# Performance work log

Hardware: AMD Instinct MI355X
Metric: run time of the kernel (lower is better)

## Reference

```python
import jax, jax.numpy as jnp
import numpy as np

B, F, V, K, D, H = 16384, 26, 100000, 16, 13, 400
IN_DIM = F * K + D  # 429
EPS = 1e-5


def _bn(x, g, b):
    # BatchNorm1d in training mode: batch statistics (biased var, like torch)
    m = jnp.mean(x, axis=0)
    v = jnp.mean((x - m) ** 2, axis=0)
    return g * (x - m) / jnp.sqrt(v + EPS) + b


def setup_inputs() -> dict:
    key = jax.random.key(0)
    ks = jax.random.split(key, 12)
    X_cat = jax.random.randint(ks[0], (B, F), 0, V)
    X_dense = jax.random.normal(ks[1], (B, D), dtype=jnp.float32)
    fm1_tables = jax.random.normal(ks[2], (F, V, 1), dtype=jnp.float32) * 0.01
    emb_tables = jax.random.normal(ks[3], (F, V, K), dtype=jnp.float32) * 0.01
    Wd = jax.random.normal(ks[4], (D, 1), dtype=jnp.float32) * 0.1
    bd = jnp.zeros((1,), jnp.float32)
    W1 = jax.random.normal(ks[5], (IN_DIM, H), dtype=jnp.float32) * (1.0 / np.sqrt(IN_DIM))
    b1 = jnp.zeros((H,), jnp.float32)
    g1 = jnp.ones((H,), jnp.float32)
    be1 = jnp.zeros((H,), jnp.float32)
    W2 = jax.random.normal(ks[6], (H, H), dtype=jnp.float32) * (1.0 / np.sqrt(H))
    b2 = jnp.zeros((H,), jnp.float32)
    g2 = jnp.ones((H,), jnp.float32)
    be2 = jnp.zeros((H,), jnp.float32)
    W3 = jax.random.normal(ks[7], (H, 1), dtype=jnp.float32) * (1.0 / np.sqrt(H))
    b3 = jnp.zeros((1,), jnp.float32)
    return dict(X_cat=X_cat, X_dense=X_dense, fm1_tables=fm1_tables,
                emb_tables=emb_tables, Wd=Wd, bd=bd, W1=W1, b1=b1, g1=g1,
                be1=be1, W2=W2, b2=b2, g2=g2, be2=be2, W3=W3, b3=b3)


def reference(X_cat, X_dense, fm1_tables, emb_tables, Wd, bd,
              W1, b1, g1, be1, W2, b2, g2, be2, W3, b3):
    gather = jax.vmap(lambda tab, idx: tab[idx], in_axes=(0, 1), out_axes=1)
    # 1st order: [B, F, 1] -> sum over fields -> [B, 1]
    y_1st = jnp.sum(gather(fm1_tables, X_cat), axis=1) + X_dense @ Wd + bd
    # 2nd order embeddings: [B, F, K]
    emb = gather(emb_tables, X_cat)
    s = jnp.sum(emb, axis=1)                 # [B, K]
    ix = s ** 2 - jnp.sum(emb ** 2, axis=1)  # [B, K]
    fm_y = 0.5 * jnp.sum(ix, axis=1, keepdims=True)
    # DNN on [flattened embeddings, dense]
    x = jnp.concatenate([emb.reshape(emb.shape[0], -1), X_dense], axis=1)
    h = jax.nn.relu(_bn(x @ W1 + b1, g1, be1))
    h = jax.nn.relu(_bn(h @ W2 + b2, g2, be2))
    dnn_y = h @ W3 + b3
    return y_1st + fm_y + dnn_y
```

## Files before the change

kernel.cpp:

```cpp
#include <hip/hip_runtime.h>
#include <stdint.h>

#define B_ROWS 16384
#define NF 26
#define NV 100000
#define ND 13
#define NH 400
#define XPAD 448
#define ZPAD 416
#define EPS 1e-5f

typedef __attribute__((ext_vector_type(8))) short short8;
typedef __attribute__((ext_vector_type(4))) float f32x4;
typedef __attribute__((ext_vector_type(4))) unsigned int uint4v;

__device__ inline float bf2f(unsigned short u) {
    union { unsigned int i; float f; } v; v.i = (unsigned int)u << 16; return v.f;
}
__device__ inline unsigned short f2bf(float f) {
    union { float f; unsigned int i; } v; v.f = f;
    unsigned int r = (v.i + 0x7fff + ((v.i >> 16) & 1)) >> 16;
    return (unsigned short)r;
}

typedef __attribute__((address_space(1))) const unsigned int g_u32;
typedef __attribute__((address_space(3))) unsigned int l_u32;
__device__ __forceinline__ void gload_lds16(const void* g, void* l) {
    __builtin_amdgcn_global_load_lds((g_u32*)g, (l_u32*)l, 16, 0, 0);
}

#define X_OFF    0
#define Z1_OFF   14680064
#define W1S_OFF  28311552
#define W2S_OFF  28712960
#define BASE_OFF 29085696
#define ST_OFF   29151232

__global__ __launch_bounds__(256) void gather_prep(
    const int* __restrict__ Xcat, const float* __restrict__ Xdense,
    const float* __restrict__ fm1, const float* __restrict__ emb,
    const float* __restrict__ Wd, const float* __restrict__ bd,
    const float* __restrict__ W1, const float* __restrict__ W2,
    unsigned short* __restrict__ X, float* __restrict__ base,
    unsigned short* __restrict__ W1s, unsigned short* __restrict__ W2s,
    float* __restrict__ st)
{
    int tid = threadIdx.x;
    if (blockIdx.x >= 1024) {
        int c = (blockIdx.x - 1024) * 256 + tid;
        if (c < 256) {
            for (int i = tid; i < 1664; i += 256) st[i] = 0.f;
        }
        const float* W; unsigned short* dst; int K; int cc;
        if (c < 25088) { W = W1; dst = W1s; K = 429; cc = c; }
        else           { W = W2; dst = W2s; K = 400; cc = c - 25088; }
        int n  = cc % 448;
        int q  = (cc / 448) & 3;
        int kt = cc / 1792;
        unsigned short o[8];
        #pragma unroll
        for (int j = 0; j < 8; ++j) {
            int k = kt * 32 + q * 8 + j;
            float v = (n < NH && k < K) ? W[(size_t)k * NH + n] : 0.f;
            o[j] = f2bf(v);
        }
        *(uint4v*)(dst + (size_t)cc * 8) = *(uint4v*)o;
        return;
    }
    int r = blockIdx.x * 16 + (tid >> 4);
    int k = tid & 15;
    const int* idxp = Xcat + (size_t)r * NF;
    unsigned short* xrow = X + (size_t)r * XPAD;

    float s = 0.f, ss = 0.f;
    #pragma unroll
    for (int f = 0; f < NF; ++f) {
        int idx = idxp[f];
        float v = emb[((size_t)f * NV + idx) * 16 + k];
        s += v; ss += v * v;
        xrow[f * 16 + k] = f2bf(v);
    }
    float fmsum = fm1[(size_t)k * NV + idxp[k]];
    if (k < NF - 16) fmsum += fm1[(size_t)(k + 16) * NV + idxp[k + 16]];
    float dsum = 0.f;
    if (k < ND) {
        float xd = Xdense[(size_t)r * ND + k];
        dsum = xd * Wd[k];
        xrow[NF * 16 + k] = f2bf(xd);
    }
    xrow[429 + k] = 0;
    if (k < 3) xrow[445 + k] = 0;

    float ix = s * s - ss;
    float rf = fmsum, rd = dsum;
    #pragma unroll
    for (int off = 8; off; off >>= 1) {
        ix += __shfl_xor(ix, off, 16);
        rf += __shfl_xor(rf, off, 16);
        rd += __shfl_xor(rd, off, 16);
    }
    if (k == 0) base[r] = 0.5f * ix + rf + rd + bd[0];
}

template<int NT, int LDA, bool APPLY_BN>
__global__ __launch_bounds__(512, 2) void mfma_gemm(
    const unsigned short* __restrict__ A,
    const unsigned short* __restrict__ Wst,
    const float* __restrict__ bias,
    const float* __restrict__ gsumIn, const float* __restrict__ gsqIn,
    const float* __restrict__ g, const float* __restrict__ be,
    unsigned short* __restrict__ Z, int ldz,
    float* __restrict__ gsum, float* __restrict__ gsq)
{
    __shared__ unsigned short b_s[2][14336];
    __shared__ float sredS[4][416];
    __shared__ float sredQ[4][416];
    __shared__ float alpha_s[416], beta_s[416];

    const int tid = threadIdx.x;
    const int lane = tid & 63;
    const int wv = tid >> 6;
    const int rowgrp = wv & 3;
    const int nhalf = wv >> 2;
    const int l15 = lane & 15;
    const int qh = lane >> 4;
    const int m0 = blockIdx.x * 64;
    const int arow = m0 + rowgrp * 16 + l15;
    const int c0 = nhalf * 208;
    const int NFRAG = nhalf ? 12 : 13;

    if constexpr (APPLY_BN) {
        for (int c = tid; c < ZPAD; c += 512) {
            float a = 0.f, b = 0.f;
            if (c < NH) {
                float mean = gsumIn[c] * (1.f / B_ROWS);
                float var  = gsqIn[c] * (1.f / B_ROWS) - mean * mean;
                a = g[c] * rsqrtf(var + EPS);
                b = be[c] - mean * a;
            }
            alpha_s[c] = a; beta_s[c] = b;
        }
    }

    f32x4 acc[13];
    #pragma unroll
    for (int i = 0; i < 13; ++i) acc[i] = f32x4{0.f, 0.f, 0.f, 0.f};

    auto stage = [&](int kt, int buf) {
        #pragma unroll
        for (int i = 0; i < 4; ++i) {
            int cchunk = wv * 256 + i * 64 + lane;
            gload_lds16(Wst + (size_t)kt * 14336 + (size_t)cchunk * 8,
                        &b_s[buf][(size_t)(wv * 256 + i * 64) * 8]);
        }
    };

    if (wv < 7) stage(0, 0);
    short8 af_next = *(const short8*)(A + (size_t)arow * LDA + qh * 8);
    __syncthreads();

    for (int kt = 0; kt < NT; ++kt) {
        if (kt + 1 < NT && wv < 7) stage(kt + 1, (kt + 1) & 1);

        short8 af = af_next;
        if (kt + 1 < NT)
            af_next = *(const short8*)(A + (size_t)arow * LDA + (kt + 1) * 32 + qh * 8);

        if constexpr (APPLY_BN) {
            const int k0 = kt * 32 + qh * 8;
            #pragma unroll
            for (int j = 0; j < 8; ++j) {
                float f = bf2f((unsigned short)af[j]);
                f = fmaxf(0.f, alpha_s[k0 + j] * f + beta_s[k0 + j]);
                af[j] = (short)f2bf(f);
            }
        }
        const unsigned short* bb = &b_s[kt & 1][(size_t)(qh * 448 + c0 + l15) * 8];
        #pragma unroll
        for (int nn = 0; nn < 13; ++nn) {
            if (nn < NFRAG) {
                short8 bf = *(const short8*)(bb + nn * 128);
                acc[nn] = __builtin_amdgcn_mfma_f32_16x16x32_bf16(af, bf, acc[nn], 0, 0, 0);
            }
        }
        __syncthreads();
    }

    #pragma unroll
    for (int nn = 0; nn < 13; ++nn) {
        if (nn < NFRAG) {
            int col = c0 + nn * 16 + l15;
            float bv = bias[col];
            float ps = 0.f, pq = 0.f;
            #pragma unroll
            for (int q = 0; q < 4; ++q) {
                float v = acc[nn][q] + bv;
                ps += v; pq += v * v;
                Z[(size_t)(m0 + rowgrp * 16 + qh * 4 + q) * ldz + col] = f2bf(v);
            }
            ps += __shfl_xor(ps, 16, 64); ps += __shfl_xor(ps, 32, 64);
            pq += __shfl_xor(pq, 16, 64); pq += __shfl_xor(pq, 32, 64);
            if (lane < 16) { sredS[rowgrp][col] = ps; sredQ[rowgrp][col] = pq; }
        }
    }
    if (nhalf == 1) {
        int col = NH + l15;
        if (col < ldz) {
            #pragma unroll
            for (int q = 0; q < 4; ++q)
                Z[(size_t)(m0 + rowgrp * 16 + qh * 4 + q) * ldz + col] = 0;
        }
    }
    __syncthreads();
    for (int c = tid; c < NH; c += 512) {
        float s = sredS[0][c] + sredS[1][c] + sredS[2][c] + sredS[3][c];
        float q = sredQ[0][c] + sredQ[1][c] + sredQ[2][c] + sredQ[3][c];
        atomicAdd(&gsum[c], s);
        atomicAdd(&gsq[c], q);
    }
}

__global__ __launch_bounds__(256) void final_kernel(
    const unsigned short* __restrict__ Z2,
    const float* __restrict__ gsum2, const float* __restrict__ gsq2,
    const float* __restrict__ g2, const float* __restrict__ be2,
    const float* __restrict__ W3, const float* __restrict__ b3,
    const float* __restrict__ base, float* __restrict__ out)
{
    __shared__ float a2s[NH], b2s[NH], w3s[NH];
    int tid = threadIdx.x;
    for (int c = tid; c < NH; c += 256) {
        float mean = gsum2[c] * (1.f / B_ROWS);
        float var  = gsq2[c] * (1.f / B_ROWS) - mean * mean;
        float a = g2[c] * rsqrtf(var + EPS);
        a2s[c] = a;
        b2s[c] = be2[c] - mean * a;
        w3s[c] = W3[c];
    }
    __syncthreads();
    int lane = tid & 63;
    int wv = tid >> 6;
    bool act = lane < 50;
    int cb = lane * 8;
    float al[8], bb[8], w3[8];
    #pragma unroll
    for (int j = 0; j < 8; ++j) {
        al[j] = act ? a2s[cb + j] : 0.f;
        bb[j] = act ? b2s[cb + j] : 0.f;
        w3[j] = act ? w3s[cb + j] : 0.f;
    }
    int r0 = blockIdx.x * 32 + wv * 8;
    float bias3 = b3[0];
    for (int t = 0; t < 8; t += 2) {
        int r = r0 + t;
        float acc0 = 0.f, acc1 = 0.f;
        if (act) {
            short8 z0 = *(const short8*)(Z2 + (size_t)r * ZPAD + cb);
            short8 z1 = *(const short8*)(Z2 + (size_t)(r + 1) * ZPAD + cb);
            #pragma unroll
            for (int j = 0; j < 8; ++j) {
                acc0 += fmaxf(0.f, al[j] * bf2f((unsigned short)z0[j]) + bb[j]) * w3[j];
                acc1 += fmaxf(0.f, al[j] * bf2f((unsigned short)z1[j]) + bb[j]) * w3[j];
            }
        }
        #pragma unroll
        for (int off = 32; off; off >>= 1) {
            acc0 += __shfl_xor(acc0, off, 64);
            acc1 += __shfl_xor(acc1, off, 64);
        }
        if (lane == 0) out[r] = base[r] + acc0 + bias3;
        if (lane == 1) out[r + 1] = base[r + 1] + acc1 + bias3;
    }
}

extern "C" void kernel_launch(void* const* d_in, const int* in_sizes, int n_in,
                              void* d_out, int out_size, void* d_ws, size_t ws_size,
                              hipStream_t stream)
{
    const int*   Xcat = (const int*)d_in[0];
    const float* Xd   = (const float*)d_in[1];
    const float* fm1  = (const float*)d_in[2];
    const float* emb  = (const float*)d_in[3];
    const float* Wd   = (const float*)d_in[4];
    const float* bd   = (const float*)d_in[5];
    const float* W1   = (const float*)d_in[6];
    const float* b1   = (const float*)d_in[7];
    const float* g1   = (const float*)d_in[8];
    const float* be1  = (const float*)d_in[9];
    const float* W2   = (const float*)d_in[10];
    const float* b2   = (const float*)d_in[11];
    const float* g2   = (const float*)d_in[12];
    const float* be2  = (const float*)d_in[13];
    const float* W3   = (const float*)d_in[14];
    const float* b3   = (const float*)d_in[15];

    char* ws = (char*)d_ws;
    unsigned short* X   = (unsigned short*)(ws + X_OFF);
    unsigned short* Z1  = (unsigned short*)(ws + Z1_OFF);
    unsigned short* Z2  = X;
    unsigned short* W1s = (unsigned short*)(ws + W1S_OFF);
    unsigned short* W2s = (unsigned short*)(ws + W2S_OFF);
    float* base = (float*)(ws + BASE_OFF);
    float* st   = (float*)(ws + ST_OFF);
    float* gsum1 = st;          float* gsq1 = st + 416;
    float* gsum2 = st + 832;    float* gsq2 = st + 1248;
    float* out = (float*)d_out;

    gather_prep<<<1213, 256, 0, stream>>>(Xcat, Xd, fm1, emb, Wd, bd, W1, W2,
                                          X, base, W1s, W2s, st);

    mfma_gemm<14, XPAD, false><<<256, 512, 0, stream>>>(
        X, W1s, b1, nullptr, nullptr, nullptr, nullptr, Z1, ZPAD, gsum1, gsq1);

    mfma_gemm<13, ZPAD, true><<<256, 512, 0, stream>>>(
        Z1, W2s, b2, gsum1, gsq1, g1, be1, Z2, ZPAD, gsum2, gsq2);

    final_kernel<<<512, 256, 0, stream>>>(Z2, gsum2, gsq2, g2, be2, W3, b3, base, out);
}
```

Before: 82.52 us.

## Fuse embedding gather into first GEMM, dropping intermediate X buffer

```diff
diff --git a/kernel.cpp b/kernel.cpp
--- a/kernel.cpp
+++ b/kernel.cpp
@@ -29,93 +29,50 @@
     __builtin_amdgcn_global_load_lds((g_u32*)g, (l_u32*)l, 16, 0, 0);
 }
 
-#define X_OFF    0
-#define Z1_OFF   14680064
-#define W1S_OFF  28311552
-#define W2S_OFF  28712960
-#define BASE_OFF 29085696
-#define ST_OFF   29151232
-
-__global__ __launch_bounds__(256) void gather_prep(
-    const int* __restrict__ Xcat, const float* __restrict__ Xdense,
-    const float* __restrict__ fm1, const float* __restrict__ emb,
-    const float* __restrict__ Wd, const float* __restrict__ bd,
+#define Z1_OFF   0
+#define Z2_OFF   13631488
+#define W1S_OFF  27262976
+#define W2S_OFF  27664384
+#define BASE_OFF 28037120
+#define ST_OFF   28102656
+
+__global__ __launch_bounds__(512) void prep_w(
     const float* __restrict__ W1, const float* __restrict__ W2,
-    unsigned short* __restrict__ X, float* __restrict__ base,
     unsigned short* __restrict__ W1s, unsigned short* __restrict__ W2s,
     float* __restrict__ st)
 {
-    int tid = threadIdx.x;
-    if (blockIdx.x >= 1024) {
-        int c = (blockIdx.x - 1024) * 256 + tid;
-        if (c < 256) {
-            for (int i = tid; i < 1664; i += 256) st[i] = 0.f;
-        }
-        const float* W; unsigned short* dst; int K; int cc;
-        if (c < 25088) { W = W1; dst = W1s; K = 429; cc = c; }
-        else           { W = W2; dst = W2s; K = 400; cc = c - 25088; }
-        int n  = cc % 448;
-        int q  = (cc / 448) & 3;
-        int kt = cc / 1792;
-        unsigned short o[8];
-        #pragma unroll
-        for (int j = 0; j < 8; ++j) {
-            int k = kt * 32 + q * 8 + j;
-            float v = (n < NH && k < K) ? W[(size_t)k * NH + n] : 0.f;
-            o[j] = f2bf(v);
-        }
-        *(uint4v*)(dst + (size_t)cc * 8) = *(uint4v*)o;
-        return;
-    }
-    int r = blockIdx.x * 16 + (tid >> 4);
-    int k = tid & 15;
-    const int* idxp = Xcat + (size_t)r * NF;
-    unsigned short* xrow = X + (size_t)r * XPAD;
-
-    float s = 0.f, ss = 0.f;
-    #pragma unroll
-    for (int f = 0; f < NF; ++f) {
-        int idx = idxp[f];
-        float v = emb[((size_t)f * NV + idx) * 16 + k];
-        s += v; ss += v * v;
-        xrow[f * 16 + k] = f2bf(v);
-    }
-    float fmsum = fm1[(size_t)k * NV + idxp[k]];
-    if (k < NF - 16) fmsum += fm1[(size_t)(k + 16) * NV + idxp[k + 16]];
-    float dsum = 0.f;
-    if (k < ND) {
-        float xd = Xdense[(size_t)r * ND + k];
-        dsum = xd * Wd[k];
-        xrow[NF * 16 + k] = f2bf(xd);
-    }
-    xrow[429 + k] = 0;
-    if (k < 3) xrow[445 + k] = 0;
-
-    float ix = s * s - ss;
-    float rf = fmsum, rd = dsum;
-    #pragma unroll
-    for (int off = 8; off; off >>= 1) {
-        ix += __shfl_xor(ix, off, 16);
-        rf += __shfl_xor(rf, off, 16);
-        rd += __shfl_xor(rd, off, 16);
-    }
-    if (k == 0) base[r] = 0.5f * ix + rf + rd + bd[0];
-}
-
-template<int NT, int LDA, bool APPLY_BN>
-__global__ __launch_bounds__(512, 2) void mfma_gemm(
-    const unsigned short* __restrict__ A,
-    const unsigned short* __restrict__ Wst,
-    const float* __restrict__ bias,
-    const float* __restrict__ gsumIn, const float* __restrict__ gsqIn,
-    const float* __restrict__ g, const float* __restrict__ be,
-    unsigned short* __restrict__ Z, int ldz,
+    int c = blockIdx.x * 512 + threadIdx.x;
+    if (blockIdx.x == 0) {
+        for (int i = threadIdx.x; i < 1664; i += 512) st[i] = 0.f;
+    }
+    if (c >= 48384) return;
+    const float* W; unsigned short* dst; int K; int cc;
+    if (c < 25088) { W = W1; dst = W1s; K = 429; cc = c; }
+    else           { W = W2; dst = W2s; K = 400; cc = c - 25088; }
+    int n  = cc % 448;
+    int q  = (cc / 448) & 3;
+    int kt = cc / 1792;
+    unsigned short o[8];
+    #pragma unroll
+    for (int j = 0; j < 8; ++j) {
+        int k = kt * 32 + q * 8 + j;
+        float v = (n < NH && k < K) ? W[(size_t)k * NH + n] : 0.f;
+        o[j] = f2bf(v);
+    }
+    *(uint4v*)(dst + (size_t)cc * 8) = *(uint4v*)o;
+}
+
+__global__ __launch_bounds__(512, 4) void gemm1_fused(
+    const int* __restrict__ Xcat, const float* __restrict__ Xd,
+    const float* __restrict__ fm1, const float* __restrict__ emb,
+    const float* __restrict__ Wd, const float* __restrict__ bd,
+    const unsigned short* __restrict__ Wst, const float* __restrict__ bias,
+    unsigned short* __restrict__ Z, float* __restrict__ base,
     float* __restrict__ gsum, float* __restrict__ gsq)
 {
     __shared__ unsigned short b_s[2][14336];
     __shared__ float sredS[4][416];
     __shared__ float sredQ[4][416];
-    __shared__ float alpha_s[416], beta_s[416];
 
     const int tid = threadIdx.x;
     const int lane = tid & 63;
@@ -129,23 +86,6 @@
     const int c0 = nhalf * 208;
     const int NFRAG = nhalf ? 12 : 13;
 
-    if constexpr (APPLY_BN) {
-        for (int c = tid; c < ZPAD; c += 512) {
-            float a = 0.f, b = 0.f;
-            if (c < NH) {
-                float mean = gsumIn[c] * (1.f / B_ROWS);
-                float var  = gsqIn[c] * (1.f / B_ROWS) - mean * mean;
-                a = g[c] * rsqrtf(var + EPS);
-                b = be[c] - mean * a;
-            }
-            alpha_s[c] = a; beta_s[c] = b;
-        }
-    }
-
-    f32x4 acc[13];
-    #pragma unroll
-    for (int i = 0; i < 13; ++i) acc[i] = f32x4{0.f, 0.f, 0.f, 0.f};
-
     auto stage = [&](int kt, int buf) {
         #pragma unroll
         for (int i = 0; i < 4; ++i) {
@@ -154,36 +94,115 @@
                         &b_s[buf][(size_t)(wv * 256 + i * 64) * 8]);
         }
     };
-
     if (wv < 7) stage(0, 0);
-    short8 af_next = *(const short8*)(A + (size_t)arow * LDA + qh * 8);
+
+    const int* idxp = Xcat + (size_t)arow * NF;
+    const int fpar = qh >> 1;
+    const int khalf = (qh & 1) << 3;
+
+    short8 fr[14];
+    float s8[8] = {0.f,0.f,0.f,0.f,0.f,0.f,0.f,0.f};
+    float ssacc = 0.f;
+    float dsum = 0.f;
+
+    {
+        float v[7][8];
+        #pragma unroll
+        for (int kt = 0; kt < 7; ++kt) {
+            int f = 2 * kt + fpar;
+            int idx = idxp[f];
+            const float* p = emb + (((size_t)f * NV + (size_t)idx) << 4) + khalf;
+            f32x4 x0 = *(const f32x4*)p;
+            f32x4 x1 = *(const f32x4*)(p + 4);
+            v[kt][0]=x0[0]; v[kt][1]=x0[1]; v[kt][2]=x0[2]; v[kt][3]=x0[3];
+            v[kt][4]=x1[0]; v[kt][5]=x1[1]; v[kt][6]=x1[2]; v[kt][7]=x1[3];
+        }
+        #pragma unroll
+        for (int kt = 0; kt < 7; ++kt) {
+            if (nhalf == 0) {
+                #pragma unroll
+                for (int j = 0; j < 8; ++j) { s8[j] += v[kt][j]; ssacc += v[kt][j]*v[kt][j]; }
+            }
+            #pragma unroll
+            for (int j = 0; j < 8; ++j) fr[kt][j] = (short)f2bf(v[kt][j]);
+        }
+    }
+    {
+        float v[7][8];
+        #pragma unroll
+        for (int kt = 7; kt < 13; ++kt) {
+            int f = 2 * kt + fpar;
+            int idx = idxp[f];
+            const float* p = emb + (((size_t)f * NV + (size_t)idx) << 4) + khalf;
+            f32x4 x0 = *(const f32x4*)p;
+            f32x4 x1 = *(const f32x4*)(p + 4);
+            v[kt-7][0]=x0[0]; v[kt-7][1]=x0[1]; v[kt-7][2]=x0[2]; v[kt-7][3]=x0[3];
+            v[kt-7][4]=x1[0]; v[kt-7][5]=x1[1]; v[kt-7][6]=x1[2]; v[kt-7][7]=x1[3];
+        }
+        #pragma unroll
+        for (int j = 0; j < 8; ++j) {
+            int cd = khalf + j;
+            v[6][j] = (qh < 2 && cd < ND) ? Xd[(size_t)arow * ND + cd] : 0.f;
+        }
+        #pragma unroll
+        for (int kt = 7; kt < 13; ++kt) {
+            if (nhalf == 0) {
+                #pragma unroll
+                for (int j = 0; j < 8; ++j) { s8[j] += v[kt-7][j]; ssacc += v[kt-7][j]*v[kt-7][j]; }
+            }
+            #pragma unroll
+            for (int j = 0; j < 8; ++j) fr[kt][j] = (short)f2bf(v[kt-7][j]);
+        }
+        #pragma unroll
+        for (int j = 0; j < 8; ++j) fr[13][j] = (short)f2bf(v[6][j]);
+        if (nhalf == 0 && qh < 2) {
+            #pragma unroll
+            for (int j = 0; j < 8; ++j) {
+                int cd = khalf + j;
+                if (cd < ND) dsum += v[6][j] * Wd[cd];
+            }
+        }
+    }
+    float fmsum = 0.f;
+    if (nhalf == 0) {
+        for (int f = qh; f < NF; f += 4)
+            fmsum += fm1[(size_t)f * NV + idxp[f]];
+    }
+
+    f32x4 acc[13];
+    #pragma unroll
+    for (int i = 0; i < 13; ++i) acc[i] = f32x4{0.f, 0.f, 0.f, 0.f};
+
     __syncthreads();
 
-    for (int kt = 0; kt < NT; ++kt) {
-        if (kt + 1 < NT && wv < 7) stage(kt + 1, (kt + 1) & 1);
-
-        short8 af = af_next;
-        if (kt + 1 < NT)
-            af_next = *(const short8*)(A + (size_t)arow * LDA + (kt + 1) * 32 + qh * 8);
-
-        if constexpr (APPLY_BN) {
-            const int k0 = kt * 32 + qh * 8;
-            #pragma unroll
-            for (int j = 0; j < 8; ++j) {
-                float f = bf2f((unsigned short)af[j]);
-                f = fmaxf(0.f, alpha_s[k0 + j] * f + beta_s[k0 + j]);
-                af[j] = (short)f2bf(f);
-            }
-        }
+    #pragma unroll
+    for (int kt = 0; kt < 14; ++kt) {
+        if (kt + 1 < 14 && wv < 7) stage(kt + 1, (kt + 1) & 1);
         const unsigned short* bb = &b_s[kt & 1][(size_t)(qh * 448 + c0 + l15) * 8];
         #pragma unroll
         for (int nn = 0; nn < 13; ++nn) {
             if (nn < NFRAG) {
                 short8 bf = *(const short8*)(bb + nn * 128);
-                acc[nn] = __builtin_amdgcn_mfma_f32_16x16x32_bf16(af, bf, acc[nn], 0, 0, 0);
+                acc[nn] = __builtin_amdgcn_mfma_f32_16x16x32_bf16(fr[kt], bf, acc[nn], 0, 0, 0);
             }
         }
         __syncthreads();
+    }
+
+    if (nhalf == 0) {
+        float red = 0.f;
+        #pragma unroll
+        for (int j = 0; j < 8; ++j) {
+            float sf = s8[j] + __shfl_xor(s8[j], 32, 64);
+            red += sf * sf;
+        }
+        red -= (ssacc + __shfl_xor(ssacc, 32, 64));
+        red += __shfl_xor(red, 16, 64);
+        float fr2 = fmsum + __shfl_xor(fmsum, 16, 64);
+        fr2 += __shfl_xor(fr2, 32, 64);
+        float dr = dsum + __shfl_xor(dsum, 16, 64);
+        dr += __shfl_xor(dr, 32, 64);
+        if (qh == 0) base[arow] = 0.5f * red + fr2 + dr + bd[0];
     }
 
     #pragma unroll
@@ -196,7 +215,7 @@
             for (int q = 0; q < 4; ++q) {
                 float v = acc[nn][q] + bv;
                 ps += v; pq += v * v;
-                Z[(size_t)(m0 + rowgrp * 16 + qh * 4 + q) * ldz + col] = f2bf(v);
+                Z[(size_t)(m0 + rowgrp * 16 + qh * 4 + q) * ZPAD + col] = f2bf(v);
             }
             ps += __shfl_xor(ps, 16, 64); ps += __shfl_xor(ps, 32, 64);
             pq += __shfl_xor(pq, 16, 64); pq += __shfl_xor(pq, 32, 64);
@@ -205,10 +224,111 @@
     }
     if (nhalf == 1) {
         int col = NH + l15;
-        if (col < ldz) {
-            #pragma unroll
-            for (int q = 0; q < 4; ++q)
-                Z[(size_t)(m0 + rowgrp * 16 + qh * 4 + q) * ldz + col] = 0;
+        #pragma unroll
+        for (int q = 0; q < 4; ++q)
+            Z[(size_t)(m0 + rowgrp * 16 + qh * 4 + q) * ZPAD + col] = 0;
+    }
+    __syncthreads();
+    for (int c = tid; c < NH; c += 512) {
+        float s = sredS[0][c] + sredS[1][c] + sredS[2][c] + sredS[3][c];
+        float q = sredQ[0][c] + sredQ[1][c] + sredQ[2][c] + sredQ[3][c];
+        atomicAdd(&gsum[c], s);
+        atomicAdd(&gsq[c], q);
+    }
+}
+
+__global__ __launch_bounds__(512, 2) void mfma_gemm2(
+    const unsigned short* __restrict__ A,
+    const unsigned short* __restrict__ Wst,
+    const float* __restrict__ bias,
+    const float* __restrict__ gsumIn, const float* __restrict__ gsqIn,
+    const float* __restrict__ g, const float* __restrict__ be,
+    unsigned short* __restrict__ Z,
+    float* __restrict__ gsum, float* __restrict__ gsq)
+{
+    __shared__ unsigned short b_s[2][14336];
+    __shared__ float sredS[4][416];
+    __shared__ float sredQ[4][416];
+    __shared__ float alpha_s[416], beta_s[416];
+
+    const int tid = threadIdx.x;
+    const int lane = tid & 63;
+    const int wv = tid >> 6;
+    const int rowgrp = wv & 3;
+    const int nhalf = wv >> 2;
+    const int l15 = lane & 15;
+    const int qh = lane >> 4;
+    const int m0 = blockIdx.x * 64;
+    const int arow = m0 + rowgrp * 16 + l15;
+    const int c0 = nhalf * 208;
+    const int NFRAG = nhalf ? 12 : 13;
+
+    for (int c = tid; c < ZPAD; c += 512) {
+        float a = 0.f, b = 0.f;
+        if (c < NH) {
+            float mean = gsumIn[c] * (1.f / B_ROWS);
+            float var  = gsqIn[c] * (1.f / B_ROWS) - mean * mean;
+            a = g[c] * rsqrtf(var + EPS);
+            b = be[c] - mean * a;
+        }
+        alpha_s[c] = a; beta_s[c] = b;
+    }
+
+    f32x4 acc[13];
+    #pragma unroll
+    for (int i = 0; i < 13; ++i) acc[i] = f32x4{0.f, 0.f, 0.f, 0.f};
+
+    auto stage = [&](int kt, int buf) {
+        #pragma unroll
+        for (int i = 0; i < 4; ++i) {
+            int cchunk = wv * 256 + i * 64 + lane;
+            gload_lds16(Wst + (size_t)kt * 14336 + (size_t)cchunk * 8,
+                        &b_s[buf][(size_t)(wv * 256 + i * 64) * 8]);
+        }
+    };
+
+    if (wv < 7) stage(0, 0);
+    short8 af_next = *(const short8*)(A + (size_t)arow * ZPAD + qh * 8);
+    __syncthreads();
+
+    for (int kt = 0; kt < 13; ++kt) {
+        if (kt + 1 < 13 && wv < 7) stage(kt + 1, (kt + 1) & 1);
+        short8 af = af_next;
+        if (kt + 1 < 13)
+            af_next = *(const short8*)(A + (size_t)arow * ZPAD + (kt + 1) * 32 + qh * 8);
+        int k0 = kt * 32 + qh * 8;
+        #pragma unroll
+        for (int j = 0; j < 8; ++j) {
+            float f = bf2f((unsigned short)af[j]);
+            f = fmaxf(0.f, alpha_s[k0 + j] * f + beta_s[k0 + j]);
+            af[j] = (short)f2bf(f);
+        }
+        const unsigned short* bb = &b_s[kt & 1][(size_t)(qh * 448 + c0 + l15) * 8];
+        #pragma unroll
+        for (int nn = 0; nn < 13; ++nn) {
+            if (nn < NFRAG) {
+                short8 bf = *(const short8*)(bb + nn * 128);
+                acc[nn] = __builtin_amdgcn_mfma_f32_16x16x32_bf16(af, bf, acc[nn], 0, 0, 0);
+            }
+        }
+        __syncthreads();
+    }
+
+    #pragma unroll
+    for (int nn = 0; nn < 13; ++nn) {
+        if (nn < NFRAG) {
+            int col = c0 + nn * 16 + l15;
+            float bv = bias[col];
+            float ps = 0.f, pq = 0.f;
+            #pragma unroll
+            for (int q = 0; q < 4; ++q) {
+                float v = acc[nn][q] + bv;
+                ps += v; pq += v * v;
+                Z[(size_t)(m0 + rowgrp * 16 + qh * 4 + q) * ZPAD + col] = f2bf(v);
+            }
+            ps += __shfl_xor(ps, 16, 64); ps += __shfl_xor(ps, 32, 64);
+            pq += __shfl_xor(pq, 16, 64); pq += __shfl_xor(pq, 32, 64);
+            if (lane < 16) { sredS[rowgrp][col] = ps; sredQ[rowgrp][col] = pq; }
         }
     }
     __syncthreads();
@@ -295,9 +415,8 @@
     const float* b3   = (const float*)d_in[15];
 
     char* ws = (char*)d_ws;
-    unsigned short* X   = (unsigned short*)(ws + X_OFF);
     unsigned short* Z1  = (unsigned short*)(ws + Z1_OFF);
-    unsigned short* Z2  = X;
+    unsigned short* Z2  = (unsigned short*)(ws + Z2_OFF);
     unsigned short* W1s = (unsigned short*)(ws + W1S_OFF);
     unsigned short* W2s = (unsigned short*)(ws + W2S_OFF);
     float* base = (float*)(ws + BASE_OFF);
@@ -306,14 +425,13 @@
     float* gsum2 = st + 832;    float* gsq2 = st + 1248;
     float* out = (float*)d_out;
 
-    gather_prep<<<1213, 256, 0, stream>>>(Xcat, Xd, fm1, emb, Wd, bd, W1, W2,
-                                          X, base, W1s, W2s, st);
-
-    mfma_gemm<14, XPAD, false><<<256, 512, 0, stream>>>(
-        X, W1s, b1, nullptr, nullptr, nullptr, nullptr, Z1, ZPAD, gsum1, gsq1);
-
-    mfma_gemm<13, ZPAD, true><<<256, 512, 0, stream>>>(
-        Z1, W2s, b2, gsum1, gsq1, g1, be1, Z2, ZPAD, gsum2, gsq2);
+    prep_w<<<95, 512, 0, stream>>>(W1, W2, W1s, W2s, st);
+
+    gemm1_fused<<<256, 512, 0, stream>>>(Xcat, Xd, fm1, emb, Wd, bd,
+                                         W1s, b1, Z1, base, gsum1, gsq1);
+
+    mfma_gemm2<<<256, 512, 0, stream>>>(Z1, W2s, b2, gsum1, gsq1, g1, be1,
+                                        Z2, gsum2, gsq2);
 
     final_kernel<<<512, 256, 0, stream>>>(Z2, gsum2, gsq2, g2, be2, W3, b3, base, out);
 }
```

After: 120.0 us. 1.45x slower.

## Restructure GEMM so each wave owns its B-slice with two row tiles, no barriers

Applied to the files above, without the earlier changes.

```diff
diff --git a/kernel.cpp b/kernel.cpp
--- a/kernel.cpp
+++ b/kernel.cpp
@@ -19,8 +19,7 @@
 }
 __device__ inline unsigned short f2bf(float f) {
     union { float f; unsigned int i; } v; v.f = f;
-    unsigned int r = (v.i + 0x7fff + ((v.i >> 16) & 1)) >> 16;
-    return (unsigned short)r;
+    return (unsigned short)((v.i + 0x7fff + ((v.i >> 16) & 1)) >> 16);
 }
 
 typedef __attribute__((address_space(1))) const unsigned int g_u32;
@@ -49,7 +48,7 @@
     if (blockIdx.x >= 1024) {
         int c = (blockIdx.x - 1024) * 256 + tid;
         if (c < 256) {
-            for (int i = tid; i < 1664; i += 256) st[i] = 0.f;
+            for (int i = tid; i < 6656; i += 256) st[i] = 0.f;
         }
         const float* W; unsigned short* dst; int K; int cc;
         if (c < 25088) { W = W1; dst = W1s; K = 429; cc = c; }
@@ -103,126 +102,127 @@
 }
 
 template<int NT, int LDA, bool APPLY_BN>
-__global__ __launch_bounds__(512, 2) void mfma_gemm(
+__global__ __launch_bounds__(512, 2) void gemm_v2(
     const unsigned short* __restrict__ A,
     const unsigned short* __restrict__ Wst,
     const float* __restrict__ bias,
-    const float* __restrict__ gsumIn, const float* __restrict__ gsqIn,
+    const float* __restrict__ st_all,
     const float* __restrict__ g, const float* __restrict__ be,
-    unsigned short* __restrict__ Z, int ldz,
-    float* __restrict__ gsum, float* __restrict__ gsq)
+    unsigned short* __restrict__ Z, int ldz, int padZ,
+    float* __restrict__ st_out, int sumOff, int sqOff)
 {
-    __shared__ unsigned short b_s[2][14336];
-    __shared__ float sredS[4][416];
-    __shared__ float sredQ[4][416];
+    __shared__ __align__(16) unsigned short slices[25600];
     __shared__ float alpha_s[416], beta_s[416];
 
-    const int tid = threadIdx.x;
-    const int lane = tid & 63;
-    const int wv = tid >> 6;
-    const int rowgrp = wv & 3;
-    const int nhalf = wv >> 2;
-    const int l15 = lane & 15;
-    const int qh = lane >> 4;
-    const int m0 = blockIdx.x * 64;
-    const int arow = m0 + rowgrp * 16 + l15;
-    const int c0 = nhalf * 208;
-    const int NFRAG = nhalf ? 12 : 13;
+    const int tid = threadIdx.x, bid = blockIdx.x;
+    const int lane = tid & 63, wv = tid >> 6;
+    const int rg = wv >> 2, w4 = wv & 3;
+    const int l15 = lane & 15, qh = lane >> 4;
+    const int cb = (w4 == 0) ? 0 : (112 + (w4 - 1) * 96);
+    const int NFW = (w4 == 0) ? 7 : 6;
+    unsigned short* slice =
+        slices + rg * 12800 + ((w4 == 0) ? 0 : (3584 + (w4 - 1) * 3072));
+    const int arowA = bid * 64 + rg * 32 + l15;
+    const int arowB = arowA + 16;
 
     if constexpr (APPLY_BN) {
         for (int c = tid; c < ZPAD; c += 512) {
             float a = 0.f, b = 0.f;
             if (c < NH) {
-                float mean = gsumIn[c] * (1.f / B_ROWS);
-                float var  = gsqIn[c] * (1.f / B_ROWS) - mean * mean;
+                float gs = 0.f, gq = 0.f;
+                #pragma unroll
+                for (int cp = 0; cp < 4; ++cp) {
+                    gs += st_all[cp * 1664 + c];
+                    gq += st_all[cp * 1664 + 416 + c];
+                }
+                float mean = gs * (1.f / 16384.f);
+                float var  = gq * (1.f / 16384.f) - mean * mean;
                 a = g[c] * rsqrtf(var + EPS);
                 b = be[c] - mean * a;
             }
             alpha_s[c] = a; beta_s[c] = b;
         }
-    }
-
-    f32x4 acc[13];
-    #pragma unroll
-    for (int i = 0; i < 13; ++i) acc[i] = f32x4{0.f, 0.f, 0.f, 0.f};
-
-    auto stage = [&](int kt, int buf) {
-        #pragma unroll
-        for (int i = 0; i < 4; ++i) {
-            int cchunk = wv * 256 + i * 64 + lane;
-            gload_lds16(Wst + (size_t)kt * 14336 + (size_t)cchunk * 8,
-                        &b_s[buf][(size_t)(wv * 256 + i * 64) * 8]);
+        __syncthreads();
+    }
+
+    f32x4 acc0[7], acc1[7];
+    #pragma unroll
+    for (int i = 0; i < 7; ++i) { acc0[i] = f32x4{0,0,0,0}; acc1[i] = f32x4{0,0,0,0}; }
+
+    auto stageW = [&](int kt) {
+        #pragma unroll
+        for (int i = 0; i < 7; ++i) if (i < NFW) {
+            int ci = (kt * 4 + qh) * 448 + cb + i * 16 + l15;
+            gload_lds16(Wst + (size_t)ci * 8, slice + i * 512);
         }
     };
 
-    if (wv < 7) stage(0, 0);
-    short8 af_next = *(const short8*)(A + (size_t)arow * LDA + qh * 8);
-    __syncthreads();
+    stageW(0);
+    short8 afA_n = *(const short8*)(A + (size_t)arowA * LDA + qh * 8);
+    short8 afB_n = *(const short8*)(A + (size_t)arowB * LDA + qh * 8);
 
     for (int kt = 0; kt < NT; ++kt) {
-        if (kt + 1 < NT && wv < 7) stage(kt + 1, (kt + 1) & 1);
-
-        short8 af = af_next;
-        if (kt + 1 < NT)
-            af_next = *(const short8*)(A + (size_t)arow * LDA + (kt + 1) * 32 + qh * 8);
-
+        asm volatile("s_waitcnt vmcnt(0)" ::: "memory");
+        __builtin_amdgcn_sched_barrier(0);
+        short8 bf[7];
+        #pragma unroll
+        for (int i = 0; i < 7; ++i) if (i < NFW)
+            bf[i] = *(const short8*)(slice + i * 512 + lane * 8);
+        short8 afA = afA_n, afB = afB_n;
+        asm volatile("s_waitcnt lgkmcnt(0)" ::: "memory");
+        __builtin_amdgcn_sched_barrier(0);
+        if (kt + 1 < NT) {
+            stageW(kt + 1);
+            afA_n = *(const short8*)(A + (size_t)arowA * LDA + (kt + 1) * 32 + qh * 8);
+            afB_n = *(const short8*)(A + (size_t)arowB * LDA + (kt + 1) * 32 + qh * 8);
+        }
         if constexpr (APPLY_BN) {
             const int k0 = kt * 32 + qh * 8;
             #pragma unroll
             for (int j = 0; j < 8; ++j) {
-                float f = bf2f((unsigned short)af[j]);
-                f = fmaxf(0.f, alpha_s[k0 + j] * f + beta_s[k0 + j]);
-                af[j] = (short)f2bf(f);
+                float fa = fmaxf(0.f, alpha_s[k0 + j] * bf2f((unsigned short)afA[j]) + beta_s[k0 + j]);
+                float fb = fmaxf(0.f, alpha_s[k0 + j] * bf2f((unsigned short)afB[j]) + beta_s[k0 + j]);
+                afA[j] = (short)f2bf(fa); afB[j] = (short)f2bf(fb);
             }
         }
-        const unsigned short* bb = &b_s[kt & 1][(size_t)(qh * 448 + c0 + l15) * 8];
-        #pragma unroll
-        for (int nn = 0; nn < 13; ++nn) {
-            if (nn < NFRAG) {
-                short8 bf = *(const short8*)(bb + nn * 128);
-                acc[nn] = __builtin_amdgcn_mfma_f32_16x16x32_bf16(af, bf, acc[nn], 0, 0, 0);
-            }
-        }
-        __syncthreads();
-    }
-
-    #pragma unroll
-    for (int nn = 0; nn < 13; ++nn) {
-        if (nn < NFRAG) {
-            int col = c0 + nn * 16 + l15;
-            float bv = bias[col];
-            float ps = 0.f, pq = 0.f;
-            #pragma unroll
-            for (int q = 0; q < 4; ++q) {
-                float v = acc[nn][q] + bv;
-                ps += v; pq += v * v;
-                Z[(size_t)(m0 + rowgrp * 16 + qh * 4 + q) * ldz + col] = f2bf(v);
-            }
-            ps += __shfl_xor(ps, 16, 64); ps += __shfl_xor(ps, 32, 64);
-            pq += __shfl_xor(pq, 16, 64); pq += __shfl_xor(pq, 32, 64);
-            if (lane < 16) { sredS[rowgrp][col] = ps; sredQ[rowgrp][col] = pq; }
-        }
-    }
-    if (nhalf == 1) {
-        int col = NH + l15;
-        if (col < ldz) {
-            #pragma unroll
-            for (int q = 0; q < 4; ++q)
-                Z[(size_t)(m0 + rowgrp * 16 + qh * 4 + q) * ldz + col] = 0;
-        }
-    }
-    __syncthreads();
-    for (int c = tid; c < NH; c += 512) {
-        float s = sredS[0][c] + sredS[1][c] + sredS[2][c] + sredS[3][c];
-        float q = sredQ[0][c] + sredQ[1][c] + sredQ[2][c] + sredQ[3][c];
-        atomicAdd(&gsum[c], s);
-        atomicAdd(&gsq[c], q);
+        #pragma unroll
+        for (int i = 0; i < 7; ++i) if (i < NFW) {
+            acc0[i] = __builtin_amdgcn_mfma_f32_16x16x32_bf16(afA, bf[i], acc0[i], 0, 0, 0);
+            acc1[i] = __builtin_amdgcn_mfma_f32_16x16x32_bf16(afB, bf[i], acc1[i], 0, 0, 0);
+        }
+    }
+
+    float* stc = st_out + (bid & 3) * 1664;
+    #pragma unroll
+    for (int i = 0; i < 7; ++i) if (i < NFW) {
+        int col = cb + i * 16 + l15;
+        float bv = bias[col];
+        float ps = 0.f, pq = 0.f;
+        #pragma unroll
+        for (int q = 0; q < 4; ++q) {
+            float v0 = acc0[i][q] + bv;
+            float v1 = acc1[i][q] + bv;
+            Z[(size_t)(bid * 64 + rg * 32 + qh * 4 + q) * ldz + col] = f2bf(v0);
+            Z[(size_t)(bid * 64 + rg * 32 + 16 + qh * 4 + q) * ldz + col] = f2bf(v1);
+            ps += v0 + v1; pq += v0 * v0 + v1 * v1;
+        }
+        ps += __shfl_xor(ps, 16, 64); ps += __shfl_xor(ps, 32, 64);
+        pq += __shfl_xor(pq, 16, 64); pq += __shfl_xor(pq, 32, 64);
+        if (qh == 0) {
+            atomicAdd(&stc[sumOff + col], ps);
+            atomicAdd(&stc[sqOff + col], pq);
+        }
+    }
+    if (padZ && w4 == 3) {
+        #pragma unroll
+        for (int rr = 0; rr < 8; ++rr)
+            Z[(size_t)(bid * 64 + rg * 32 + rr * 4 + qh) * ldz + 400 + l15] = 0;
     }
 }
 
 __global__ __launch_bounds__(256) void final_kernel(
     const unsigned short* __restrict__ Z2,
-    const float* __restrict__ gsum2, const float* __restrict__ gsq2,
+    const float* __restrict__ st_all,
     const float* __restrict__ g2, const float* __restrict__ be2,
     const float* __restrict__ W3, const float* __restrict__ b3,
     const float* __restrict__ base, float* __restrict__ out)
@@ -230,8 +230,14 @@
     __shared__ float a2s[NH], b2s[NH], w3s[NH];
     int tid = threadIdx.x;
     for (int c = tid; c < NH; c += 256) {
-        float mean = gsum2[c] * (1.f / B_ROWS);
-        float var  = gsq2[c] * (1.f / B_ROWS) - mean * mean;
+        float gs = 0.f, gq = 0.f;
+        #pragma unroll
+        for (int cp = 0; cp < 4; ++cp) {
+            gs += st_all[cp * 1664 + 832 + c];
+            gq += st_all[cp * 1664 + 1248 + c];
+        }
+        float mean = gs * (1.f / 16384.f);
+        float var  = gq * (1.f / 16384.f) - mean * mean;
         float a = g2[c] * rsqrtf(var + EPS);
         a2s[c] = a;
         b2s[c] = be2[c] - mean * a;
@@ -302,18 +308,16 @@
     unsigned short* W2s = (unsigned short*)(ws + W2S_OFF);
     float* base = (float*)(ws + BASE_OFF);
     float* st   = (float*)(ws + ST_OFF);
-    float* gsum1 = st;          float* gsq1 = st + 416;
-    float* gsum2 = st + 832;    float* gsq2 = st + 1248;
-    float* out = (float*)d_out;
+    float* out  = (float*)d_out;
 
     gather_prep<<<1213, 256, 0, stream>>>(Xcat, Xd, fm1, emb, Wd, bd, W1, W2,
                                           X, base, W1s, W2s, st);
 
-    mfma_gemm<14, XPAD, false><<<256, 512, 0, stream>>>(
-        X, W1s, b1, nullptr, nullptr, nullptr, nullptr, Z1, ZPAD, gsum1, gsq1);
-
-    mfma_gemm<13, ZPAD, true><<<256, 512, 0, stream>>>(
-        Z1, W2s, b2, gsum1, gsq1, g1, be1, Z2, ZPAD, gsum2, gsq2);
-
-    final_kernel<<<512, 256, 0, stream>>>(Z2, gsum2, gsq2, g2, be2, W3, b3, base, out);
-}
+    gemm_v2<14, XPAD, false><<<256, 512, 0, stream>>>(
+        X, W1s, b1, nullptr, nullptr, nullptr, Z1, ZPAD, 1, st, 0, 416);
+
+    gemm_v2<13, ZPAD, true><<<256, 512, 0, stream>>>(
+        Z1, W2s, b2, st, g1, be1, Z2, ZPAD, 0, st, 832, 1248);
+
+    final_kernel<<<512, 256, 0, stream>>>(Z2, st, g2, be2, W3, b3, base, out);
+}
```

Result: faster. 73.48 us (-11.0%).
